# Performance work log

Measured on AMD Instinct MI355X. Metric: run time of the kernel, lower is better.

## Reference

```python
import jax, jax.numpy as jnp
from jax import lax
import numpy as np

D_MODEL = 512
D_PROJ = 256
PATCH = 4
NL = 8
D_STATE = 16
D_CONV = 4
EXPAND = 2
D_INNER = EXPAND * D_MODEL          # 1024
DT_RANK = (D_MODEL + 15) // 16      # 32
B = 4
SEQ = 1024
NF = 1
EPS = 1e-5


def setup_inputs() -> dict:
    key = jax.random.key(0)
    ks = jax.random.split(key, 12)
    s = 0.02
    def rn(k, shape):
        return jax.random.normal(k, shape, jnp.float32) * s
    A_init = jnp.log(jnp.arange(1, D_STATE + 1, dtype=jnp.float32))  # (n,)
    return {
        "time_series": jax.random.normal(ks[0], (B, SEQ, NF), jnp.float32),
        "mask": jnp.ones((B, SEQ), jnp.int32),
        "emb_w": rn(ks[1], (D_MODEL, PATCH)),
        "emb_b": jnp.zeros((D_MODEL,), jnp.float32),
        "norm_w": jnp.ones((NL, D_MODEL), jnp.float32),
        "in_w": rn(ks[2], (NL, 2, 2 * D_INNER, D_MODEL)),
        "conv_w": rn(ks[3], (NL, 2, D_INNER, D_CONV)),
        "conv_b": jnp.zeros((NL, 2, D_INNER), jnp.float32),
        "xproj_w": rn(ks[4], (NL, 2, DT_RANK + 2 * D_STATE, D_INNER)),
        "dt_w": rn(ks[5], (NL, 2, D_INNER, DT_RANK)),
        "dt_b": jnp.full((NL, 2, D_INNER), float(np.log(np.expm1(0.01))), jnp.float32),
        "A_log": jnp.broadcast_to(A_init, (NL, 2, D_INNER, D_STATE)) + jnp.zeros((NL, 2, D_INNER, D_STATE), jnp.float32),
        "Dp": jnp.ones((NL, 2, D_INNER), jnp.float32),
        "out_w": rn(ks[6], (NL, 2, D_MODEL, D_INNER)),
        "proj_w": rn(ks[7], (PATCH * D_PROJ, D_MODEL)),
        "proj_b": jnp.zeros((PATCH * D_PROJ,), jnp.float32),
    }


def rmsnorm(x, w):
    return x * lax.rsqrt(jnp.mean(x * x, axis=-1, keepdims=True) + EPS) * w


def mamba(x, in_w, conv_w, conv_b, xproj_w, dt_w, dt_b, A_log, Dp, out_w):
    # x: (B, L, D_MODEL)
    Bsz, L, _ = x.shape
    xz = jnp.einsum('bld,ed->ble', x, in_w)                 # (B,L,2*d_inner)
    u, z = jnp.split(xz, 2, axis=-1)                         # each (B,L,d_inner)
    # depthwise causal conv1d along L
    u_t = jnp.transpose(u, (0, 2, 1))                        # (B,d_inner,L)
    u_pad = jnp.pad(u_t, ((0, 0), (0, 0), (D_CONV - 1, 0)))
    conv = lax.conv_general_dilated(
        u_pad, conv_w[:, None, :], window_strides=(1,), padding='VALID',
        feature_group_count=D_INNER, dimension_numbers=('NCH', 'OIH', 'NCH'))
    u = jax.nn.silu(jnp.transpose(conv + conv_b[None, :, None], (0, 2, 1)))  # (B,L,d_inner)
    x_dbl = jnp.einsum('ble,re->blr', u, xproj_w)            # (B,L,dt_rank+2n)
    dt, Bm, C = jnp.split(x_dbl, [DT_RANK, DT_RANK + D_STATE], axis=-1)
    delta = jax.nn.softplus(jnp.einsum('blr,er->ble', dt, dt_w) + dt_b)  # (B,L,d_inner)
    A = -jnp.exp(A_log)                                      # (d_inner,n)

    def step(h, inp):
        d_t, B_t, C_t, u_t = inp                             # (B,e),(B,n),(B,n),(B,e)
        dA = jnp.exp(d_t[..., None] * A)                     # (B,e,n)
        h = dA * h + (d_t * u_t)[..., None] * B_t[:, None, :]
        y = jnp.einsum('ben,bn->be', h, C_t)
        return h, y

    h0 = jnp.zeros((Bsz, D_INNER, D_STATE), x.dtype)
    xs = (jnp.moveaxis(delta, 1, 0), jnp.moveaxis(Bm, 1, 0),
          jnp.moveaxis(C, 1, 0), jnp.moveaxis(u, 1, 0))
    _, ys = lax.scan(step, h0, xs)                           # ys: (L,B,e)
    y = jnp.moveaxis(ys, 0, 1) + u * Dp
    y = y * jax.nn.silu(z)
    return jnp.einsum('ble,de->bld', y, out_w)               # (B,L,D_MODEL)


def reference(time_series, mask, emb_w, emb_b, norm_w, in_w, conv_w, conv_b,
              xproj_w, dt_w, dt_b, A_log, Dp, out_w, proj_w, proj_b):
    Bsz, S, F_ = time_series.shape
    NP = S // PATCH  # S is a multiple of PATCH
    patches = time_series.reshape(Bsz, NP, PATCH, F_)
    patches = jnp.transpose(patches, (0, 3, 1, 2)).reshape(Bsz, F_ * NP, PATCH)
    x = patches @ emb_w.T + emb_b                            # (B, F*NP, D_MODEL)
    for i in range(NL):
        res = x
        xn = rmsnorm(x, norm_w[i])
        yf = mamba(xn, in_w[i, 0], conv_w[i, 0], conv_b[i, 0], xproj_w[i, 0],
                   dt_w[i, 0], dt_b[i, 0], A_log[i, 0], Dp[i, 0], out_w[i, 0])
        yb = mamba(jnp.flip(xn, axis=1), in_w[i, 1], conv_w[i, 1], conv_b[i, 1],
                   xproj_w[i, 1], dt_w[i, 1], dt_b[i, 1], A_log[i, 1], Dp[i, 1], out_w[i, 1])
        x = yf + jnp.flip(yb, axis=1) + res
    proj = x @ proj_w.T + proj_b                             # (B, F*NP, PATCH*D_PROJ)
    le = proj.reshape(Bsz, F_, NP, PATCH, D_PROJ)
    le = jnp.transpose(le, (0, 2, 3, 1, 4)).reshape(Bsz, NP * PATCH, F_, D_PROJ)
    return le[:, :S]
```

## Files before the change

kernel.cpp:

```cpp
#include <hip/hip_runtime.h>
#include <hip/hip_bf16.h>

#define DM 512
#define DI 1024
#define DSTATE 16
#define DTR 32
#define NLAYER 8
#define BS 4
#define LL 256
#define MT 1024
#define DPROJ 256

typedef unsigned short u16;
typedef unsigned int u32;
typedef __attribute__((ext_vector_type(8))) short short8;
typedef __attribute__((ext_vector_type(4))) float f32x4;

__device__ __forceinline__ float sigmoidf_(float x){ return 1.f/(1.f+__expf(-x)); }

__device__ __forceinline__ u16 f2bf(float f){
  unsigned u = __float_as_uint(f);
  u = (u + 0x7FFF + ((u>>16)&1)) >> 16;
  return (u16)u;
}
__device__ __forceinline__ float bf2f(u16 v){
  return __uint_as_float(((unsigned)v) << 16);
}

template<int CTRL>
__device__ __forceinline__ float dpp_ror_add(float x){
  int y = __builtin_amdgcn_update_dpp(0, __float_as_int(x), CTRL, 0xF, 0xF, false);
  return x + __int_as_float(y);
}
__device__ __forceinline__ float sum16_dpp(float x){
  x = dpp_ror_add<0x128>(x);
  x = dpp_ror_add<0x124>(x);
  x = dpp_ror_add<0x122>(x);
  x = dpp_ror_add<0x121>(x);
  return x;
}

__global__ __launch_bounds__(256) void embed_k(const float* __restrict__ ts,
    const float* __restrict__ ew, const float* __restrict__ eb, float* __restrict__ x){
  int idx = blockIdx.x*256 + threadIdx.x;
  int m = idx >> 9, d = idx & 511;
  int b = m >> 8, np_ = m & 255;
  const float* t0 = ts + b*1024 + np_*4;
  float acc = eb[d];
  #pragma unroll
  for (int p=0;p<4;p++) acc = fmaf(t0[p], ew[d*4+p], acc);
  x[idx] = acc;
}

__global__ __launch_bounds__(256) void wcastall_k(
    const float* __restrict__ w_in, const float* __restrict__ w_out,
    const float* __restrict__ w_xp, const float* __restrict__ w_pj,
    u16* __restrict__ dst){
  int t = blockIdx.x*256 + threadIdx.x;
  long e4 = (long)t*4;
  const float* src; long o;
  if      (e4 < 16777216) { src = w_in;  o = e4; }
  else if (e4 < 25165824) { src = w_out; o = e4 - 16777216; }
  else if (e4 < 26214400) { src = w_xp;  o = e4 - 25165824; }
  else                    { src = w_pj;  o = e4 - 26214400; }
  float4 v = *(const float4*)(src + o);
  ushort4 r; r.x=f2bf(v.x); r.y=f2bf(v.y); r.z=f2bf(v.z); r.w=f2bf(v.w);
  *(ushort4*)(dst + e4) = r;
}

__global__ __launch_bounds__(256) void rmscomb_k(float* __restrict__ x,
    const float* __restrict__ yout,
    const float* __restrict__ nw, u16* __restrict__ xnbf, u16* __restrict__ xnfbf){
  int m = blockIdx.x, t = threadIdx.x;
  int b = m>>8, l = m&255, mf = (b<<8)+(255-l);
  float2 v = *(const float2*)&x[(long)m*DM + t*2];
  if (yout){
    float2 f = *(const float2*)&yout[(long)m*DM + t*2];
    float2 g = *(const float2*)&yout[(long)MT*DM + (long)mf*DM + t*2];
    v.x += f.x + g.x; v.y += f.y + g.y;
    *(float2*)&x[(long)m*DM + t*2] = v;
  }
  float ss = v.x*v.x + v.y*v.y;
  ss += __shfl_down(ss,32); ss += __shfl_down(ss,16); ss += __shfl_down(ss,8);
  ss += __shfl_down(ss,4);  ss += __shfl_down(ss,2);  ss += __shfl_down(ss,1);
  __shared__ float ps[4];
  if ((t&63)==0) ps[t>>6] = ss;
  __syncthreads();
  float tot = ps[0]+ps[1]+ps[2]+ps[3];
  float rs = rsqrtf(tot*(1.f/DM) + 1e-5f);
  ushort2 o; o.x = f2bf(v.x*rs*nw[t*2]); o.y = f2bf(v.y*rs*nw[t*2+1]);
  *(ushort2*)&xnbf [(long)m *DM + t*2] = o;
  *(ushort2*)&xnfbf[(long)mf*DM + t*2] = o;
}

__global__ __launch_bounds__(256) void combcast_k(const float* __restrict__ x,
    const float* __restrict__ yout, u16* __restrict__ xbf){
  int idx = blockIdx.x*256 + threadIdx.x;
  int m = idx >> 7, c4 = idx & 127;
  int b = m>>8, l = m&255, mf = (b<<8)+(255-l);
  float4 r = ((const float4*)x)[idx];
  float4 f = ((const float4*)yout)[idx];
  float4 g = ((const float4*)(yout + (long)MT*DM))[(long)mf*128 + c4];
  ushort4 o;
  o.x = f2bf(r.x + f.x + g.x); o.y = f2bf(r.y + f.y + g.y);
  o.z = f2bf(r.z + f.z + g.z); o.w = f2bf(r.w + f.w + g.w);
  ((ushort4*)xbf)[idx] = o;
}

template<int BM,int BN,int SPLITK,int EPI>
__global__ __launch_bounds__(256) void mfma_nt(
    const u16* __restrict__ A, int lda, long sA,
    const u16* __restrict__ W, int ldw, long sW,
    const float* __restrict__ bias, u16* __restrict__ G,
    float* __restrict__ C, int ldc, long sC,
    int M, int N, int K)
{
  constexpr int WM = BM/2, WN = BN/2;
  constexpr int MI = WM/16, NI = WN/16;
  int z = blockIdx.z;
  int dir = z / SPLITK, kc = z % SPLITK;
  int Klen = K / SPLITK;
  int kbase = kc * Klen;
  A += (long)dir * sA;
  W += (long)dir * sW;
  if (SPLITK > 1) C += (long)z * M * N; else C += (long)dir * sC;
  if (EPI==4) G += (long)dir * (long)MT*DI;

  __shared__ u16 Al[BM*32];
  __shared__ u16 Wl[BN*32];
  int tid = threadIdx.x;
  int lane = tid & 63;
  int wave = tid >> 6;
  int wm0 = (wave>>1)*WM, wn0 = (wave&1)*WN;
  int m0 = blockIdx.y*BM, n0 = blockIdx.x*BN;
  int l16 = lane>>4, l15 = lane&15;

  f32x4 acc[MI][NI] = {};

  for (int k0=0; k0<Klen; k0+=32){
    #pragma unroll
    for (int it=0; it<BM*4/256; ++it){
      int ch = it*256 + tid;
      int row = ch % BM, kk = ch / BM;
      const u16* g = A + (long)(m0+row)*lda + kbase + k0 + kk*8;
      __builtin_amdgcn_global_load_lds(
          (const __attribute__((address_space(1))) void*)g,
          (__attribute__((address_space(3))) void*)(Al + ch*8), 16, 0, 0);
    }
    #pragma unroll
    for (int it=0; it<BN*4/256; ++it){
      int ch = it*256 + tid;
      int row = ch % BN, kk = ch / BN;
      const u16* g = W + (long)(n0+row)*ldw + kbase + k0 + kk*8;
      __builtin_amdgcn_global_load_lds(
          (const __attribute__((address_space(1))) void*)g,
          (__attribute__((address_space(3))) void*)(Wl + ch*8), 16, 0, 0);
    }
    __syncthreads();
    short8 a[MI], b[NI];
    #pragma unroll
    for (int i=0;i<MI;i++)
      a[i] = *(const short8*)&Al[(l16*BM + wm0 + i*16 + l15)*8];
    #pragma unroll
    for (int j=0;j<NI;j++)
      b[j] = *(const short8*)&Wl[(l16*BN + wn0 + j*16 + l15)*8];
    #pragma unroll
    for (int i=0;i<MI;i++)
      #pragma unroll
      for (int j=0;j<NI;j++)
        acc[i][j] = __builtin_amdgcn_mfma_f32_16x16x32_bf16(a[i], b[j], acc[i][j], 0,0,0);
    __syncthreads();
  }
  #pragma unroll
  for (int i=0;i<MI;i++){
    #pragma unroll
    for (int j=0;j<NI;j++){
      #pragma unroll
      for (int r=0;r<4;r++){
        int m = m0 + wm0 + i*16 + l16*4 + r;
        int n = n0 + wn0 + j*16 + l15;
        float v = acc[i][j][r];
        if (EPI==2){
          v += bias[n];
          int bb = m>>8, np_ = m&255, p = n>>8, dp = n&255;
          C[((long)(bb*1024 + np_*4 + p))*256 + dp] = v;
        } else if (EPI==4){
          if (n < 1024) C[(long)m*1024 + n] = v;
          else          G[(long)m*1024 + (n-1024)] = f2bf(v * sigmoidf_(v));
        } else {
          C[(long)m*ldc + n] = v;
        }
      }
    }
  }
}

__global__ __launch_bounds__(256) void xreduce_k(const float* __restrict__ part,
    float* __restrict__ xdbl){
  int idx = blockIdx.x*256 + threadIdx.x;
  int d = idx >> 16, off = idx & 65535;
  float s = 0.f;
  #pragma unroll
  for (int kc=0; kc<8; ++kc) s += part[((d*8+kc)<<16) + off];
  xdbl[idx] = s;
}

__global__ __launch_bounds__(256) void conv_silu_k(const float* __restrict__ xzu,
    const float* __restrict__ cw, const float* __restrict__ cb,
    u16* __restrict__ ubf){
  int idx = blockIdx.x*256 + threadIdx.x;
  int e = idx & (DI-1);
  int grp = idx >> 10;
  int dir = grp >> 8;
  int b   = (grp >> 6) & 3;
  int l0  = (grp & 63) * 4;
  long dm0 = (long)dir*MT + b*LL + l0;
  const float* w = cw + ((long)dir*DI + e)*4;
  float w0=w[0], w1=w[1], w2=w[2], w3=w[3];
  float bias = cb[dir*DI + e];
  const float* src = xzu + dm0*DI + e;
  float vb[7];
  #pragma unroll
  for (int j=0;j<7;j++){
    int l = l0 - 3 + j;
    vb[j] = (l >= 0) ? src[(long)(j-3)*DI] : 0.f;
  }
  #pragma unroll
  for (int j=0;j<4;j++){
    float acc = bias;
    acc = fmaf(w0, vb[j],   acc);
    acc = fmaf(w1, vb[j+1], acc);
    acc = fmaf(w2, vb[j+2], acc);
    acc = fmaf(w3, vb[j+3], acc);
    float v = acc * sigmoidf_(acc);
    ubf[(dm0+j)*DI + e] = f2bf(v);
  }
}

__global__ __launch_bounds__(64) void scan_k(
    const u16* __restrict__ ubf, const u16* __restrict__ gbf,
    const float* __restrict__ xdbl, const float* __restrict__ dtw,
    const float* __restrict__ dtb, const float* __restrict__ A_log,
    const float* __restrict__ Dp, u16* __restrict__ ygbf)
{
  int t = threadIdx.x;
  int n = t & 15, g = t >> 4;
  int id = blockIdx.x + 256*blockIdx.y + 1024*blockIdx.z;
  int xcd = id & 7, s = id >> 3;
  int ecb = xcd*32 + (s & 31);
  int rest = s >> 5;
  int b = rest & 3, dir = rest >> 2;
  int e0 = ecb*4;

  long mbase = (long)dir*MT + b*LL;
  const u16* up_ = ubf + mbase*DI + e0;
  const u16* gp_ = gbf + mbase*DI + e0;
  const float* xd_ = xdbl + mbase*64;
  u16* yp_ = ygbf + mbase*DI + e0;

  float Av = -__expf(A_log[((long)dir*DI + e0 + g)*16 + n]);
  float Dv = Dp[dir*DI + e0 + g];

  float wrow[32];
  {
    const float* wr = dtw + ((long)dir*DI + e0 + g)*32;
    #pragma unroll
    for (int r4=0;r4<8;r4++) *(float4*)&wrow[r4*4] = *(const float4*)&wr[r4*4];
  }
  float dtbv = dtb[dir*DI + e0 + g];

  __shared__ u32 sDU[32][4][2];
  __shared__ u32 sBC[32][20];
  __shared__ float sy[32][4];

  ushort4 ru, rg;
  float4 rb0, rb1, rc0, rc1;
  int brow = t >> 1, bseg = t & 1;

  auto loadrg = [&](int c){
    int l0 = c*32;
    if (t < 32){
      ru = *(const ushort4*)&up_[(long)(l0 + t)*DI];
      rg = *(const ushort4*)&gp_[(long)(l0 + t)*DI];
    }
    const float* src = &xd_[(long)(l0 + brow)*64 + 32 + bseg*8];
    rb0 = *(const float4*)&src[0];
    rb1 = *(const float4*)&src[4];
    rc0 = *(const float4*)&src[16];
    rc1 = *(const float4*)&src[20];
  };

  loadrg(0);
  float h = 0.f;

  for (int c = 0; c < 8; ++c){
    int l0 = c*32;
    if (t < 32){
      sDU[t][0][1] = ru.x; sDU[t][1][1] = ru.y;
      sDU[t][2][1] = ru.z; sDU[t][3][1] = ru.w;
    }
    {
      uint4 p0, p1;
      p0.x = (u32)f2bf(rb0.x) | ((u32)f2bf(rc0.x)<<16);
      p0.y = (u32)f2bf(rb0.y) | ((u32)f2bf(rc0.y)<<16);
      p0.z = (u32)f2bf(rb0.z) | ((u32)f2bf(rc0.z)<<16);
      p0.w = (u32)f2bf(rb0.w) | ((u32)f2bf(rc0.w)<<16);
      p1.x = (u32)f2bf(rb1.x) | ((u32)f2bf(rc1.x)<<16);
      p1.y = (u32)f2bf(rb1.y) | ((u32)f2bf(rc1.y)<<16);
      p1.z = (u32)f2bf(rb1.z) | ((u32)f2bf(rc1.z)<<16);
      p1.w = (u32)f2bf(rb1.w) | ((u32)f2bf(rc1.w)<<16);
      *(uint4*)&sBC[brow][bseg*8]     = p0;
      *(uint4*)&sBC[brow][bseg*8 + 4] = p1;
    }
    #pragma unroll
    for (int j=0;j<2;j++){
      int l = n + j*16;
      const float* row = &xd_[(long)(l0 + l)*64];
      float acc = dtbv;
      #pragma unroll
      for (int r4=0;r4<8;r4++){
        float4 d4 = *(const float4*)&row[r4*4];
        acc = fmaf(d4.x, wrow[r4*4],   acc);
        acc = fmaf(d4.y, wrow[r4*4+1], acc);
        acc = fmaf(d4.z, wrow[r4*4+2], acc);
        acc = fmaf(d4.w, wrow[r4*4+3], acc);
      }
      acc = fmaxf(acc, 0.f) + __logf(1.f + __expf(-fabsf(acc)));
      sDU[l][g][0] = __float_as_uint(acc);
    }
    ushort4 gcur = rg;
    __syncthreads();
    if (c < 7) loadrg(c+1);

    #pragma unroll 8
    for (int l = 0; l < 32; ++l){
      uint2 du = *(const uint2*)&sDU[l][g][0];
      float dv = __uint_as_float(du.x);
      float uv = bf2f((u16)du.y);
      u32 bc = sBC[l][n];
      float Bv = bf2f((u16)(bc & 0xffff));
      float Cv = bf2f((u16)(bc >> 16));
      float dA = __expf(dv*Av);
      h = fmaf(dA, h, dv*uv*Bv);
      float yc = sum16_dpp(h*Cv);
      if (n==0) sy[l][g] = yc + uv*Dv;
    }
    __builtin_amdgcn_wave_barrier();

    if (t < 32){
      float4 y4 = *(const float4*)&sy[t][0];
      ushort4 o;
      o.x = f2bf(y4.x * bf2f(gcur.x)); o.y = f2bf(y4.y * bf2f(gcur.y));
      o.z = f2bf(y4.z * bf2f(gcur.z)); o.w = f2bf(y4.w * bf2f(gcur.w));
      *(ushort4*)&yp_[(long)(l0 + t)*DI] = o;
    }
    __syncthreads();
  }
}

extern "C" void kernel_launch(void* const* d_in, const int* in_sizes, int n_in,
                              void* d_out, int out_size, void* d_ws, size_t ws_size,
                              hipStream_t stream){
  const float* ts   = (const float*)d_in[0];
  const float* ew   = (const float*)d_in[2];
  const float* eb   = (const float*)d_in[3];
  const float* nw   = (const float*)d_in[4];
  const float* inw  = (const float*)d_in[5];
  const float* cw   = (const float*)d_in[6];
  const float* cb   = (const float*)d_in[7];
  const float* xpw  = (const float*)d_in[8];
  const float* dtw  = (const float*)d_in[9];
  const float* dtb  = (const float*)d_in[10];
  const float* alog = (const float*)d_in[11];
  const float* dpp  = (const float*)d_in[12];
  const float* outw = (const float*)d_in[13];
  const float* pw   = (const float*)d_in[14];
  const float* pb   = (const float*)d_in[15];
  float* out = (float*)d_out;

  float* ws   = (float*)d_ws;
  float* x    = ws;
  float* xzu  = ws + 524288;
  float* xdbl = ws + 2621440;
  float* yout = ws + 2752512;
  float* xpart= ws + 3801088;
  u16* ub     = (u16*)(ws + 4849664);
  u16* xn_bf  = ub;
  u16* u_bf   = ub + 1048576;
  u16* g_bf   = ub + 3145728;
  u16* yg_bf  = ub + 5242880;
  u16* x_bf   = ub + 7340032;
  u16* wb     = ub + 7864320;
  u16* wb_in  = wb;
  u16* wb_out = wb + 16777216;
  u16* wb_xp  = wb + 25165824;
  u16* wb_pj  = wb + 26214400;

  dim3 blk(256);

  embed_k<<<MT*DM/256, blk, 0, stream>>>(ts, ew, eb, x);
  wcastall_k<<<26112, blk, 0, stream>>>(inw, outw, xpw, pw, wb);

  for (int i=0;i<NLAYER;i++){
    rmscomb_k<<<MT, blk, 0, stream>>>(x, i ? yout : nullptr, nw + i*DM,
        xn_bf, xn_bf + MT*DM);
    mfma_nt<64,128,1,4><<<dim3(16,16,2), blk, 0, stream>>>(
        xn_bf, DM, (long)MT*DM, wb_in + (long)i*2097152, DM, 1048576,
        nullptr, g_bf, xzu, 1024, (long)MT*1024, MT, 2048, DM);
    conv_silu_k<<<2048, blk, 0, stream>>>(xzu, cw + (long)i*2*DI*4, cb + i*2*DI, u_bf);
    mfma_nt<64,64,8,0><<<dim3(1,16,16), blk, 0, stream>>>(
        u_bf, DI, (long)MT*DI, wb_xp + (long)i*131072, DI, 65536,
        nullptr, nullptr, xpart, 64, 0, MT, 64, DI);
    xreduce_k<<<512, blk, 0, stream>>>(xpart, xdbl);
    scan_k<<<dim3(256, BS, 2), dim3(64), 0, stream>>>(u_bf, g_bf, xdbl,
        dtw + (long)i*2*DI*DTR, dtb + (long)i*2*DI,
        alog + (long)i*2*DI*16, dpp + i*2*DI, yg_bf);
    mfma_nt<64,64,1,0><<<dim3(8,16,2), blk, 0, stream>>>(
        yg_bf, DI, (long)MT*DI, wb_out + (long)i*1048576, DI, 524288,
        nullptr, nullptr, yout, DM, (long)MT*DM, MT, DM, DI);
  }
  combcast_k<<<MT*DM/4/256, blk, 0, stream>>>(x, yout, x_bf);
  mfma_nt<64,64,1,2><<<dim3(16,16,1), blk, 0, stream>>>(
      x_bf, DM, 0, wb_pj, DM, 0, pb, nullptr, out, 1024, 0, MT, 1024, DM);
}
```

Before: 870.3 us.

## Transpose scan shared-memory layout and split recurrence into batched vectorized phases

Transposes the shared buffers for delta/u and B/C so each thread can read its 32-step chunk with wide vector loads instead of per-step scalar loads. The scan loop is split into separate phases: precompute exp and input terms, run the serial recurrence with only one FMA per step, then apply the C multiply and the DPP reductions in batch. This shortens the loop-carried dependency chain and lets the independent reductions overlap. The cost is much higher register pressure (several 32-element arrays per thread) and bank conflicts on the transposed stores.

```diff
diff --git a/kernel.cpp b/kernel.cpp
--- a/kernel.cpp
+++ b/kernel.cpp
@@ -269,8 +269,8 @@
   }
   float dtbv = dtb[dir*DI + e0 + g];
 
-  __shared__ u32 sDU[32][4][2];
-  __shared__ u32 sBC[32][20];
+  __shared__ u32 sDU[4][80];
+  __shared__ u32 sBC[16][36];
   __shared__ float sy[32][4];
 
   ushort4 ru, rg;
@@ -296,21 +296,21 @@
   for (int c = 0; c < 8; ++c){
     int l0 = c*32;
     if (t < 32){
-      sDU[t][0][1] = ru.x; sDU[t][1][1] = ru.y;
-      sDU[t][2][1] = ru.z; sDU[t][3][1] = ru.w;
+      sDU[0][2*t+1] = ru.x; sDU[1][2*t+1] = ru.y;
+      sDU[2][2*t+1] = ru.z; sDU[3][2*t+1] = ru.w;
     }
     {
-      uint4 p0, p1;
-      p0.x = (u32)f2bf(rb0.x) | ((u32)f2bf(rc0.x)<<16);
-      p0.y = (u32)f2bf(rb0.y) | ((u32)f2bf(rc0.y)<<16);
-      p0.z = (u32)f2bf(rb0.z) | ((u32)f2bf(rc0.z)<<16);
-      p0.w = (u32)f2bf(rb0.w) | ((u32)f2bf(rc0.w)<<16);
-      p1.x = (u32)f2bf(rb1.x) | ((u32)f2bf(rc1.x)<<16);
-      p1.y = (u32)f2bf(rb1.y) | ((u32)f2bf(rc1.y)<<16);
-      p1.z = (u32)f2bf(rb1.z) | ((u32)f2bf(rc1.z)<<16);
-      p1.w = (u32)f2bf(rb1.w) | ((u32)f2bf(rc1.w)<<16);
-      *(uint4*)&sBC[brow][bseg*8]     = p0;
-      *(uint4*)&sBC[brow][bseg*8 + 4] = p1;
+      u32 pb[8];
+      pb[0] = (u32)f2bf(rb0.x) | ((u32)f2bf(rc0.x)<<16);
+      pb[1] = (u32)f2bf(rb0.y) | ((u32)f2bf(rc0.y)<<16);
+      pb[2] = (u32)f2bf(rb0.z) | ((u32)f2bf(rc0.z)<<16);
+      pb[3] = (u32)f2bf(rb0.w) | ((u32)f2bf(rc0.w)<<16);
+      pb[4] = (u32)f2bf(rb1.x) | ((u32)f2bf(rc1.x)<<16);
+      pb[5] = (u32)f2bf(rb1.y) | ((u32)f2bf(rc1.y)<<16);
+      pb[6] = (u32)f2bf(rb1.z) | ((u32)f2bf(rc1.z)<<16);
+      pb[7] = (u32)f2bf(rb1.w) | ((u32)f2bf(rc1.w)<<16);
+      #pragma unroll
+      for (int k=0;k<8;k++) sBC[bseg*8 + k][brow] = pb[k];
     }
     #pragma unroll
     for (int j=0;j<2;j++){
@@ -326,24 +326,46 @@
         acc = fmaf(d4.w, wrow[r4*4+3], acc);
       }
       acc = fmaxf(acc, 0.f) + __logf(1.f + __expf(-fabsf(acc)));
-      sDU[l][g][0] = __float_as_uint(acc);
+      sDU[g][2*l] = __float_as_uint(acc);
     }
     ushort4 gcur = rg;
     __syncthreads();
     if (c < 7) loadrg(c+1);
 
-    #pragma unroll 8
-    for (int l = 0; l < 32; ++l){
-      uint2 du = *(const uint2*)&sDU[l][g][0];
-      float dv = __uint_as_float(du.x);
-      float uv = bf2f((u16)du.y);
-      u32 bc = sBC[l][n];
-      float Bv = bf2f((u16)(bc & 0xffff));
-      float Cv = bf2f((u16)(bc >> 16));
-      float dA = __expf(dv*Av);
-      h = fmaf(dA, h, dv*uv*Bv);
-      float yc = sum16_dpp(h*Cv);
-      if (n==0) sy[l][g] = yc + uv*Dv;
+    float dA[32], sv[32], ud[32];
+    u32  bcp[32];
+    {
+      const u32* pdu = &sDU[g][0];
+      const u32* pbc = &sBC[n][0];
+      #pragma unroll
+      for (int l4=0; l4<8; ++l4){
+        uint4 a0 = *(const uint4*)&pdu[l4*8];
+        uint4 a1 = *(const uint4*)&pdu[l4*8+4];
+        uint4 bc = *(const uint4*)&pbc[l4*4];
+        int L = l4*4;
+        float dv0 = __uint_as_float(a0.x), uv0 = bf2f((u16)a0.y);
+        float dv1 = __uint_as_float(a0.z), uv1 = bf2f((u16)a0.w);
+        float dv2 = __uint_as_float(a1.x), uv2 = bf2f((u16)a1.y);
+        float dv3 = __uint_as_float(a1.z), uv3 = bf2f((u16)a1.w);
+        dA[L  ] = __expf(dv0*Av); sv[L  ] = dv0*uv0*bf2f((u16)(bc.x & 0xffff)); ud[L  ] = uv0*Dv;
+        dA[L+1] = __expf(dv1*Av); sv[L+1] = dv1*uv1*bf2f((u16)(bc.y & 0xffff)); ud[L+1] = uv1*Dv;
+        dA[L+2] = __expf(dv2*Av); sv[L+2] = dv2*uv2*bf2f((u16)(bc.z & 0xffff)); ud[L+2] = uv2*Dv;
+        dA[L+3] = __expf(dv3*Av); sv[L+3] = dv3*uv3*bf2f((u16)(bc.w & 0xffff)); ud[L+3] = uv3*Dv;
+        bcp[L] = bc.x; bcp[L+1] = bc.y; bcp[L+2] = bc.z; bcp[L+3] = bc.w;
+      }
+    }
+    #pragma unroll
+    for (int l=0; l<32; ++l){
+      h = fmaf(dA[l], h, sv[l]);
+      sv[l] = h;
+    }
+    #pragma unroll
+    for (int l=0; l<32; ++l) sv[l] *= bf2f((u16)(bcp[l] >> 16));
+    #pragma unroll
+    for (int l=0; l<32; ++l) sv[l] = sum16_dpp(sv[l]);
+    if (n == 0){
+      #pragma unroll
+      for (int l=0; l<32; ++l) sy[l][g] = sv[l] + ud[l];
     }
     __builtin_amdgcn_wave_barrier();
 
```

Result: faster. 824.6 us (-5.2%).
